# Performance work log

Measured on AMD Instinct MI355X. Metric: run time of the kernel, lower is better.

## Reference

```python
import jax, jax.numpy as jnp
import numpy as np

N_FFT = 1024
N_STAGES = 3
S = 2 ** N_STAGES          # 8 leaf subsequences
LEAF = N_FFT // S          # 128-point dense leaf DFT
BATCH = 32768


def _quant8(w):
    # torch quant8: fake-quantize to int8 grid with power-of-2 scale, split into upper+lower
    mv = np.abs(w).max()
    q = np.ceil(np.log2(mv)) - 6.0
    upper = np.round(w / 2.0 ** q) * 2.0 ** q
    return upper.astype(np.float32), (w - upper).astype(np.float32)


def setup_inputs() -> dict:
    key = jax.random.key(0)
    x = jax.random.normal(key, (BATCH, N_FFT), dtype=jnp.float32)
    k = np.arange(LEAF)
    theta = -2.0 * np.pi * np.outer(k, k) / LEAF  # forward DFT: exp(-2*pi*i*k*n/N)
    fft_real = np.cos(theta)
    fft_imag = np.sin(theta)
    fr_u, fr_l = _quant8(fft_real)
    fi_u, fi_l = _quant8(fft_imag)
    return {
        "x": x,
        "fr_u": jnp.asarray(fr_u), "fr_l": jnp.asarray(fr_l),
        "fi_u": jnp.asarray(fi_u), "fi_l": jnp.asarray(fi_l),
    }


def reference(x, fr_u, fr_l, fi_u, fi_l):
    # bit-reversed stride offsets for decimation-in-time leaves
    offsets = [int(format(j, '0%db' % N_STAGES)[::-1], 2) for j in range(S)]
    xs = jnp.stack([x[..., o::S] for o in offsets], axis=0)  # [S, B, LEAF]
    # leaf dense DFT as two split-precision GEMMs (virtual int16)
    real = jnp.einsum('gbn,kn->gbk', xs, fr_u) + jnp.einsum('gbn,kn->gbk', xs, fr_l)
    imag = jnp.einsum('gbn,kn->gbk', xs, fi_u) + jnp.einsum('gbn,kn->gbk', xs, fi_l)
    # radix-2 twiddle combine stages
    for _ in range(N_STAGES):
        G, B, size = real.shape
        k = jnp.arange(size, dtype=jnp.float32)
        th = -2.0 * jnp.pi * k / (2.0 * size)
        c, s = jnp.cos(th), jnp.sin(th)
        r2 = real.reshape(G // 2, 2, B, size)
        i2 = imag.reshape(G // 2, 2, B, size)
        ev_r, od_r = r2[:, 0], r2[:, 1]
        ev_i, od_i = i2[:, 0], i2[:, 1]
        t_r = c * od_r - s * od_i  # twiddle complex multiply
        t_i = c * od_i + s * od_r
        real = jnp.concatenate([ev_r + t_r, ev_r - t_r], axis=-1)
        imag = jnp.concatenate([ev_i + t_i, ev_i - t_i], axis=-1)
    return real[0], imag[0]
```

## Files before the change

kernel.cpp:

```cpp
#include <hip/hip_runtime.h>
#include <hip/hip_bf16.h>
#include <math.h>

typedef __bf16 bf16x8 __attribute__((ext_vector_type(8)));
typedef unsigned short u16x8 __attribute__((ext_vector_type(8)));
typedef float f32x4 __attribute__((ext_vector_type(4)));

#define BATCH 32768
#define NFFT 1024
#define LDA 136
#define ROWS_PER_WG 16
#define TWO_PI 6.283185307179586f

__device__ __forceinline__ unsigned short f2bf(float f) {
    __hip_bfloat16 h = __float2bfloat16(f);
    return __builtin_bit_cast(unsigned short, h);
}

__global__ void build_w(const float* __restrict__ fru, const float* __restrict__ frl,
                        const float* __restrict__ fiu, const float* __restrict__ fil,
                        __hip_bfloat16* __restrict__ Wc, __hip_bfloat16* __restrict__ Ws)
{
    int i = blockIdx.x * 256 + threadIdx.x;
    if (i < 128 * 128) {
        Wc[i] = __float2bfloat16(fru[i] + frl[i]);
        Ws[i] = __float2bfloat16(fiu[i] + fil[i]);
    }
}

__global__ __launch_bounds__(256, 2)
void fft_main(const float* __restrict__ x,
              const __hip_bfloat16* __restrict__ Wc,
              const __hip_bfloat16* __restrict__ Ws,
              float* __restrict__ outR,
              float* __restrict__ outI)
{
    __shared__ unsigned short As[128 * LDA];

    const int t = threadIdx.x;
    const int rowbase = blockIdx.x * ROWS_PER_WG;

    {
        const int m = t >> 1;
        const int h = t & 1;
        const int brow = m >> 3;
        const int g = m & 7;
        const int o = ((g & 1) << 2) | (g & 2) | ((g & 4) >> 2);
        const float* xr = x + (size_t)(rowbase + brow) * NFFT + o;
        #pragma unroll
        for (int jj = 0; jj < 8; ++jj) {
            u16x8 v;
            #pragma unroll
            for (int j = 0; j < 8; ++j)
                v[j] = f2bf(xr[(h * 64 + jj * 8 + j) * 8]);
            *(u16x8*)&As[m * LDA + h * 64 + jj * 8] = v;
        }
    }
    __syncthreads();

    const int wave = t >> 6;
    const int lane = t & 63;
    const int wr = wave >> 1;
    const int wc = wave & 1;
    const int lcol = lane & 15;
    const int quad = lane >> 4;

    f32x4 accR[4][4], accI[4][4];
    #pragma unroll
    for (int i = 0; i < 4; ++i)
        #pragma unroll
        for (int j = 0; j < 4; ++j) { accR[i][j] = (f32x4)0.0f; accI[i][j] = (f32x4)0.0f; }

    const unsigned short* WcU = (const unsigned short*)Wc;
    const unsigned short* WsU = (const unsigned short*)Ws;

    #pragma unroll
    for (int ko = 0; ko < 4; ++ko) {
        bf16x8 af[4];
        #pragma unroll
        for (int rt = 0; rt < 4; ++rt) {
            u16x8 a = *(const u16x8*)&As[(wr * 64 + rt * 16 + lcol) * LDA + ko * 32 + quad * 8];
            af[rt] = __builtin_bit_cast(bf16x8, a);
        }
        #pragma unroll
        for (int nt = 0; nt < 4; ++nt) {
            const int kcol = wc * 64 + nt * 16 + lcol;
            bf16x8 bc = __builtin_bit_cast(bf16x8, *(const u16x8*)&WcU[kcol * 128 + ko * 32 + quad * 8]);
            bf16x8 bs = __builtin_bit_cast(bf16x8, *(const u16x8*)&WsU[kcol * 128 + ko * 32 + quad * 8]);
            #pragma unroll
            for (int rt = 0; rt < 4; ++rt) {
                accR[rt][nt] = __builtin_amdgcn_mfma_f32_16x16x32_bf16(af[rt], bc, accR[rt][nt], 0, 0, 0);
                accI[rt][nt] = __builtin_amdgcn_mfma_f32_16x16x32_bf16(af[rt], bs, accI[rt][nt], 0, 0, 0);
            }
        }
    }

    #pragma unroll
    for (int nt = 0; nt < 4; ++nt) {
        const int kk = wc * 64 + nt * 16 + lcol;
        float c1, s1, c2a, s2a, c2b, s2b;
        __sincosf(-TWO_PI * (float)kk * (1.0f / 256.0f), &s1, &c1);
        __sincosf(-TWO_PI * (float)kk * (1.0f / 512.0f), &s2a, &c2a);
        __sincosf(-TWO_PI * (float)(kk + 128) * (1.0f / 512.0f), &s2b, &c2b);
        float c3[4], s3[4];
        #pragma unroll
        for (int r = 0; r < 4; ++r)
            __sincosf(-TWO_PI * (float)(kk + 128 * r) * (1.0f / 1024.0f), &s3[r], &c3[r]);

        #pragma unroll
        for (int rt = 0; rt < 4; ++rt) {
            float R[4], I[4];
            #pragma unroll
            for (int r = 0; r < 4; ++r) { R[r] = accR[rt][nt][r]; I[r] = accI[rt][nt][r]; }

            {
                float tr = c1 * R[1] - s1 * I[1], ti = c1 * I[1] + s1 * R[1];
                float er = R[0], ei = I[0];
                R[0] = er + tr; I[0] = ei + ti; R[1] = er - tr; I[1] = ei - ti;
                tr = c1 * R[3] - s1 * I[3]; ti = c1 * I[3] + s1 * R[3];
                er = R[2]; ei = I[2];
                R[2] = er + tr; I[2] = ei + ti; R[3] = er - tr; I[3] = ei - ti;
            }
            {
                float tr = c2a * R[2] - s2a * I[2], ti = c2a * I[2] + s2a * R[2];
                float er = R[0], ei = I[0];
                R[0] = er + tr; I[0] = ei + ti; R[2] = er - tr; I[2] = ei - ti;
                tr = c2b * R[3] - s2b * I[3]; ti = c2b * I[3] + s2b * R[3];
                er = R[1]; ei = I[1];
                R[1] = er + tr; I[1] = ei + ti; R[3] = er - tr; I[3] = ei - ti;
            }
            const bool evq = (quad & 1) == 0;
            #pragma unroll
            for (int r = 0; r < 4; ++r) {
                float pr = __shfl_xor(R[r], 16, 64);
                float pi = __shfl_xor(I[r], 16, 64);
                float Rres, Ires;
                if (evq) {
                    float tr = c3[r] * pr - s3[r] * pi;
                    float ti = c3[r] * pi + s3[r] * pr;
                    Rres = R[r] + tr; Ires = I[r] + ti;
                } else {
                    float tr = c3[r] * R[r] - s3[r] * I[r];
                    float ti = c3[r] * I[r] + s3[r] * R[r];
                    Rres = pr - tr; Ires = pi - ti;
                }
                const int mloc = wr * 64 + rt * 16 + quad * 4 + r;
                const int brow = rowbase + (mloc >> 3);
                const int g = mloc & 7;
                const size_t idx = (size_t)brow * NFFT + g * 128 + kk;
                outR[idx] = Rres;
                outI[idx] = Ires;
            }
        }
    }
}

extern "C" void kernel_launch(void* const* d_in, const int* in_sizes, int n_in,
                              void* d_out, int out_size, void* d_ws, size_t ws_size,
                              hipStream_t stream)
{
    const float* x   = (const float*)d_in[0];
    const float* fru = (const float*)d_in[1];
    const float* frl = (const float*)d_in[2];
    const float* fiu = (const float*)d_in[3];
    const float* fil = (const float*)d_in[4];

    __hip_bfloat16* Wc = (__hip_bfloat16*)d_ws;
    __hip_bfloat16* Ws = Wc + 128 * 128;

    float* outR = (float*)d_out;
    float* outI = outR + (size_t)BATCH * NFFT;

    build_w<<<64, 256, 0, stream>>>(fru, frl, fiu, fil, Wc, Ws);
    fft_main<<<BATCH / ROWS_PER_WG, 256, 0, stream>>>(x, Wc, Ws, outR, outI);
}
```

Before: 410.7 us.

## Coalesce input loads, restructure GEMM per column tile, raise occupancy

The input staging now reads contiguous float4 chunks per thread and scatters bf16 pairs into the bit-reversed LDS layout, replacing strided scalar global loads. The GEMM loop is reordered so each column tile (nt) accumulates only 8 accumulators and is immediately followed by the twiddle epilogue, cutting register pressure so launch bounds can request 4 workgroups per CU. Twiddles for earlier stages are derived from the final-stage sincos via double-angle identities, reducing transcendental calls. The trade-off is reloading A fragments from LDS for every column tile and small precision differences in the derived twiddles.

```diff
diff --git a/kernel.cpp b/kernel.cpp
--- a/kernel.cpp
+++ b/kernel.cpp
@@ -12,11 +12,6 @@
 #define ROWS_PER_WG 16
 #define TWO_PI 6.283185307179586f
 
-__device__ __forceinline__ unsigned short f2bf(float f) {
-    __hip_bfloat16 h = __float2bfloat16(f);
-    return __builtin_bit_cast(unsigned short, h);
-}
-
 __global__ void build_w(const float* __restrict__ fru, const float* __restrict__ frl,
                         const float* __restrict__ fiu, const float* __restrict__ fil,
                         __hip_bfloat16* __restrict__ Wc, __hip_bfloat16* __restrict__ Ws)
@@ -28,7 +23,7 @@
     }
 }
 
-__global__ __launch_bounds__(256, 2)
+__global__ __launch_bounds__(256, 4)
 void fft_main(const float* __restrict__ x,
               const __hip_bfloat16* __restrict__ Wc,
               const __hip_bfloat16* __restrict__ Ws,
@@ -40,20 +35,25 @@
     const int t = threadIdx.x;
     const int rowbase = blockIdx.x * ROWS_PER_WG;
 
-    {
-        const int m = t >> 1;
-        const int h = t & 1;
-        const int brow = m >> 3;
-        const int g = m & 7;
-        const int o = ((g & 1) << 2) | (g & 2) | ((g & 4) >> 2);
-        const float* xr = x + (size_t)(rowbase + brow) * NFFT + o;
+    #pragma unroll
+    for (int it = 0; it < 4; ++it) {
+        const int q    = it * 256 + t;
+        const int brow = q >> 6;
+        const int c64  = q & 63;
+        const float* p = x + (size_t)(rowbase + brow) * NFFT + c64 * 16;
+        float4 v0 = *(const float4*)(p);
+        float4 v1 = *(const float4*)(p + 4);
+        float4 v2 = *(const float4*)(p + 8);
+        float4 v3 = *(const float4*)(p + 12);
+        float lo[8] = {v0.x, v0.y, v0.z, v0.w, v1.x, v1.y, v1.z, v1.w};
+        float hi[8] = {v2.x, v2.y, v2.z, v2.w, v3.x, v3.y, v3.z, v3.w};
+        const int ncol = c64 * 2;
         #pragma unroll
-        for (int jj = 0; jj < 8; ++jj) {
-            u16x8 v;
-            #pragma unroll
-            for (int j = 0; j < 8; ++j)
-                v[j] = f2bf(xr[(h * 64 + jj * 8 + j) * 8]);
-            *(u16x8*)&As[m * LDA + h * 64 + jj * 8] = v;
+        for (int e = 0; e < 8; ++e) {
+            const int g = ((e & 1) << 2) | (e & 2) | ((e & 4) >> 2);
+            const int m = brow * 8 + g;
+            __hip_bfloat162 pk = __float22bfloat162_rn(make_float2(lo[e], hi[e]));
+            *(__hip_bfloat162*)&As[m * LDA + ncol] = pk;
         }
     }
     __syncthreads();
@@ -65,53 +65,43 @@
     const int lcol = lane & 15;
     const int quad = lane >> 4;
 
-    f32x4 accR[4][4], accI[4][4];
-    #pragma unroll
-    for (int i = 0; i < 4; ++i)
-        #pragma unroll
-        for (int j = 0; j < 4; ++j) { accR[i][j] = (f32x4)0.0f; accI[i][j] = (f32x4)0.0f; }
-
     const unsigned short* WcU = (const unsigned short*)Wc;
     const unsigned short* WsU = (const unsigned short*)Ws;
 
-    #pragma unroll
-    for (int ko = 0; ko < 4; ++ko) {
-        bf16x8 af[4];
+    #pragma unroll 1
+    for (int nt = 0; nt < 4; ++nt) {
+        f32x4 accR[4], accI[4];
         #pragma unroll
-        for (int rt = 0; rt < 4; ++rt) {
-            u16x8 a = *(const u16x8*)&As[(wr * 64 + rt * 16 + lcol) * LDA + ko * 32 + quad * 8];
-            af[rt] = __builtin_bit_cast(bf16x8, a);
-        }
+        for (int i = 0; i < 4; ++i) { accR[i] = (f32x4)0.0f; accI[i] = (f32x4)0.0f; }
+
+        const int kk = wc * 64 + nt * 16 + lcol;
+
         #pragma unroll
-        for (int nt = 0; nt < 4; ++nt) {
-            const int kcol = wc * 64 + nt * 16 + lcol;
-            bf16x8 bc = __builtin_bit_cast(bf16x8, *(const u16x8*)&WcU[kcol * 128 + ko * 32 + quad * 8]);
-            bf16x8 bs = __builtin_bit_cast(bf16x8, *(const u16x8*)&WsU[kcol * 128 + ko * 32 + quad * 8]);
+        for (int ko = 0; ko < 4; ++ko) {
+            bf16x8 bc = __builtin_bit_cast(bf16x8, *(const u16x8*)&WcU[kk * 128 + ko * 32 + quad * 8]);
+            bf16x8 bs = __builtin_bit_cast(bf16x8, *(const u16x8*)&WsU[kk * 128 + ko * 32 + quad * 8]);
             #pragma unroll
             for (int rt = 0; rt < 4; ++rt) {
-                accR[rt][nt] = __builtin_amdgcn_mfma_f32_16x16x32_bf16(af[rt], bc, accR[rt][nt], 0, 0, 0);
-                accI[rt][nt] = __builtin_amdgcn_mfma_f32_16x16x32_bf16(af[rt], bs, accI[rt][nt], 0, 0, 0);
+                u16x8 a = *(const u16x8*)&As[(wr * 64 + rt * 16 + lcol) * LDA + ko * 32 + quad * 8];
+                bf16x8 af = __builtin_bit_cast(bf16x8, a);
+                accR[rt] = __builtin_amdgcn_mfma_f32_16x16x32_bf16(af, bc, accR[rt], 0, 0, 0);
+                accI[rt] = __builtin_amdgcn_mfma_f32_16x16x32_bf16(af, bs, accI[rt], 0, 0, 0);
             }
         }
-    }
 
-    #pragma unroll
-    for (int nt = 0; nt < 4; ++nt) {
-        const int kk = wc * 64 + nt * 16 + lcol;
-        float c1, s1, c2a, s2a, c2b, s2b;
-        __sincosf(-TWO_PI * (float)kk * (1.0f / 256.0f), &s1, &c1);
-        __sincosf(-TWO_PI * (float)kk * (1.0f / 512.0f), &s2a, &c2a);
-        __sincosf(-TWO_PI * (float)(kk + 128) * (1.0f / 512.0f), &s2b, &c2b);
         float c3[4], s3[4];
         #pragma unroll
         for (int r = 0; r < 4; ++r)
             __sincosf(-TWO_PI * (float)(kk + 128 * r) * (1.0f / 1024.0f), &s3[r], &c3[r]);
+        const float c2a = c3[0] * c3[0] - s3[0] * s3[0], s2a = 2.0f * c3[0] * s3[0];
+        const float c2b = c3[1] * c3[1] - s3[1] * s3[1], s2b = 2.0f * c3[1] * s3[1];
+        const float c1  = c2a * c2a - s2a * s2a,         s1  = 2.0f * c2a * s2a;
 
         #pragma unroll
         for (int rt = 0; rt < 4; ++rt) {
             float R[4], I[4];
             #pragma unroll
-            for (int r = 0; r < 4; ++r) { R[r] = accR[rt][nt][r]; I[r] = accI[rt][nt][r]; }
+            for (int r = 0; r < 4; ++r) { R[r] = accR[rt][r]; I[r] = accI[rt][r]; }
 
             {
                 float tr = c1 * R[1] - s1 * I[1], ti = c1 * I[1] + s1 * R[1];
```

New measurement: 426.2 us. +3.8%, slower.
